# Kernel tuning notes

Hardware: AMD Instinct MI355X
Metric: run time of the kernel (lower is better)

The kernel has to match this reference:

```python
import jax, jax.numpy as jnp
import numpy as np

GRID_SIZE = 10
DEGREE = 3


def bspline_basis(x, grid_size=GRID_SIZE, degree=DEGREE):
    """Cox-de Boor B-spline basis on a uniform grid over [-1, 1].
    x: (...,) -> (..., grid_size + degree)
    """
    h = 2.0 / grid_size
    # extended knot vector, length grid_size + 2*degree + 1
    knots = jnp.arange(-degree, grid_size + degree + 1, dtype=x.dtype) * h - 1.0
    # keep inputs inside the grid support (standard KAN practice)
    x = jnp.clip(x, -1.0, 1.0 - 1e-6)
    xe = x[..., None]
    b = ((xe >= knots[:-1]) & (xe < knots[1:])).astype(x.dtype)  # degree-0, (..., K-1)
    for d in range(1, degree + 1):
        left = (xe - knots[: -(d + 1)]) / (knots[d:-1] - knots[: -(d + 1)]) * b[..., :-1]
        right = (knots[d + 1:] - xe) / (knots[d + 1:] - knots[1:-d]) * b[..., 1:]
        b = left + right
    return b  # (..., grid_size + degree)


def setup_inputs() -> dict:
    key = jax.random.key(0)
    k1, k2, k3 = jax.random.split(key, 3)
    B, S, IN, OUT, E = 4, 2048, 256, 256, 8
    n_basis = GRID_SIZE + DEGREE
    x = jax.random.normal(k1, (B, S, IN), dtype=jnp.float32)
    coeff = jax.random.normal(k2, (E, n_basis), dtype=jnp.float32) * 0.1
    gating_weights = jax.random.normal(k3, (IN, OUT, E), dtype=jnp.float32)
    return {"x": x, "coeff": coeff, "gating_weights": gating_weights}


def reference(x, coeff, gating_weights):
    # spline experts: elementwise basis eval, then per-expert linear combo
    basis = bspline_basis(x)                              # (B, S, I, n_basis)
    expert_outputs = jnp.einsum('bsin,en->bsie', basis, coeff)  # (B, S, I, E)
    gates = jax.nn.softmax(gating_weights, axis=-1)       # (I, O, E)
    out = jnp.einsum('bsie,ioe->bso', expert_outputs, gates)
    return out
```

## Files before the change

### kernel.cpp

```cpp
#include <hip/hip_runtime.h>

typedef __attribute__((ext_vector_type(8))) short short8;
typedef __attribute__((ext_vector_type(4))) float f32x4;

#define IN_DIM 256
#define OUT_DIM 256
#define NB 16
#define KDIM (IN_DIM * NB)
#define TM 128
#define TN 128
#define BK 64
#define LDA 72
#define KSPLIT 4
#define IPER (IN_DIM / KSPLIT)
#define STEPS (IPER / 4)

__device__ __forceinline__ unsigned short f2bf(float f) {
  union { float f; unsigned int u; } v; v.f = f;
  unsigned int r = v.u + 0x7fffu + ((v.u >> 16) & 1u);
  return (unsigned short)(r >> 16);
}

__device__ __forceinline__ void spline_row(float xv, unsigned short* rowp) {
  float xc = fminf(fmaxf(xv, -1.0f), 1.0f - 1e-6f);
  float u = (xc + 1.0f) * 5.0f;
  int c = (int)u;
  c = c > 9 ? 9 : (c < 0 ? 0 : c);
  float tt = u - (float)c;
  float omt = 1.0f - tt;
  float t2 = tt * tt, t3 = t2 * tt;
  float b0 = omt * omt * omt * (1.0f / 6.0f);
  float b1 = (3.0f * t3 - 6.0f * t2 + 4.0f) * (1.0f / 6.0f);
  float b2 = (-3.0f * t3 + 3.0f * t2 + 3.0f * tt + 1.0f) * (1.0f / 6.0f);
  float b3 = t3 * (1.0f / 6.0f);
  unsigned h0 = f2bf(b0), h1 = f2bf(b1), h2 = f2bf(b2), h3 = f2bf(b3);
  const int a = c >> 1;
  const bool odd = (c & 1) != 0;
  unsigned p01 = h0 | (h1 << 16);
  unsigned p23 = h2 | (h3 << 16);
  unsigned A0 = odd ? (h0 << 16) : p01;
  unsigned A1 = odd ? (h1 | (h2 << 16)) : p23;
  unsigned A2 = odd ? h3 : 0u;
  unsigned d[8];
#pragma unroll
  for (int j = 0; j < 8; ++j) {
    unsigned v = (j == a) ? A0 : 0u;
    v = (j == a + 1) ? A1 : v;
    v = (j == a + 2) ? A2 : v;
    d[j] = v;
  }
  *(int4*)&rowp[0] = *(const int4*)&d[0];
  *(int4*)&rowp[8] = *(const int4*)&d[4];
}

__global__ __launch_bounds__(256) void kan_prep(const float* __restrict__ coeff,
                                                const float* __restrict__ gw,
                                                unsigned short* __restrict__ BmT,
                                                float* __restrict__ out) {
  __shared__ float csh[104];
  __shared__ unsigned short tile[16][256];
  const int t = threadIdx.x;
  {
    const int bid = blockIdx.y * 16 + blockIdx.x;
    float4 z; z.x = z.y = z.z = z.w = 0.f;
    float4* ob = (float4*)out;
#pragma unroll
    for (int j = 0; j < 8; ++j) ob[(size_t)bid * 2048 + j * 256 + t] = z;
  }
  if (t < 104) csh[t] = coeff[t];
  __syncthreads();
  const int otile = blockIdx.x, itile = blockIdx.y;
  const int il = t >> 4, ol = t & 15;
  const int i = itile * 16 + il;
  const int o = otile * 16 + ol;
  const float* g = gw + (size_t)(i * OUT_DIM + o) * 8;
  float4 g0 = *(const float4*)g;
  float4 g1 = *(const float4*)(g + 4);
  float ge[8] = {g0.x, g0.y, g0.z, g0.w, g1.x, g1.y, g1.z, g1.w};
  float mx = ge[0];
#pragma unroll
  for (int e = 1; e < 8; ++e) mx = fmaxf(mx, ge[e]);
  float p[8]; float s = 0.f;
#pragma unroll
  for (int e = 0; e < 8; ++e) { p[e] = __expf(ge[e] - mx); s += p[e]; }
  const float inv = 1.0f / s;
  unsigned short row[16];
#pragma unroll
  for (int n = 0; n < 13; ++n) {
    float w = 0.f;
#pragma unroll
    for (int e = 0; e < 8; ++e) w += p[e] * csh[e * 13 + n];
    row[n] = f2bf(w * inv);
  }
  row[13] = 0; row[14] = 0; row[15] = 0;
  int4* dst = (int4*)&tile[ol][il * 16];
  dst[0] = *(const int4*)&row[0];
  dst[1] = *(const int4*)&row[8];
  __syncthreads();
  const int oo = t >> 4, ck = t & 15;
  int4 v0 = *(const int4*)&tile[oo][ck * 16];
  int4 v1 = *(const int4*)&tile[oo][ck * 16 + 8];
  int4* out4 = (int4*)(BmT + (size_t)(otile * 16 + oo) * KDIM + itile * 256 + ck * 16);
  out4[0] = v0;
  out4[1] = v1;
}

__global__ __launch_bounds__(256, 2) void kan_gemm(const float* __restrict__ x,
                                                   const unsigned short* __restrict__ BmT,
                                                   float* __restrict__ out) {
  __shared__ unsigned short AshB[2][TM * LDA];
  __shared__ unsigned short BshB[2][TN * LDA];

  const int t = threadIdx.x;
  const int lane = t & 63;
  const int wave = t >> 6;
  const int wm = wave & 1, wn = wave >> 1;
  const int mb = blockIdx.x * TM;
  const int ob = blockIdx.y * TN;
  const int i0 = blockIdx.z * IPER;

  const int r = t & 127;
  const int ph = t >> 7;
  const float* xrow = x + (size_t)(mb + r) * IN_DIM + i0 + 2 * ph;
  const int adst = r * LDA + 2 * ph * NB;

  const unsigned short* bsrc[4];
  int bdst[4];
#pragma unroll
  for (int q = 0; q < 4; ++q) {
    int olo = (t >> 3) + 32 * q;
    bsrc[q] = BmT + (size_t)(ob + olo) * KDIM + i0 * NB + (t & 7) * 8;
    bdst[q] = olo * LDA + (t & 7) * 8;
  }

  f32x4 acc[4][4];
#pragma unroll
  for (int a = 0; a < 4; ++a)
#pragma unroll
    for (int b = 0; b < 4; ++b) acc[a][b] = (f32x4){0.f, 0.f, 0.f, 0.f};

  int aoff[4], boff[4];
#pragma unroll
  for (int f = 0; f < 4; ++f) {
    aoff[f] = (wm * 64 + f * 16 + (lane & 15)) * LDA + (lane >> 4) * 8;
    boff[f] = (wn * 64 + f * 16 + (lane & 15)) * LDA + (lane >> 4) * 8;
  }

  float2 xs[STEPS];
#pragma unroll
  for (int s = 0; s < STEPS; ++s) xs[s] = *(const float2*)(xrow + 4 * s);

  {
    int4 breg[4];
#pragma unroll
    for (int q = 0; q < 4; ++q) breg[q] = *(const int4*)(bsrc[q]);
#pragma unroll
    for (int q = 0; q < 4; ++q) *(int4*)&BshB[0][bdst[q]] = breg[q];
    spline_row(xs[0].x, &AshB[0][adst]);
    spline_row(xs[0].y, &AshB[0][adst + NB]);
  }

#pragma unroll
  for (int s = 0; s < STEPS; ++s) {
    __syncthreads();
    const int cur = s & 1;
    const bool more = (s + 1 < STEPS);
    int4 breg[4];
    if (more) {
#pragma unroll
      for (int q = 0; q < 4; ++q) breg[q] = *(const int4*)(bsrc[q] + (s + 1) * BK);
    }
    const unsigned short* Ac = AshB[cur];
    const unsigned short* Bc = BshB[cur];
#pragma unroll
    for (int kc = 0; kc < 2; ++kc) {
      short8 af[4], bfr[4];
#pragma unroll
      for (int f = 0; f < 4; ++f) af[f] = *(const short8*)&Ac[aoff[f] + kc * 32];
#pragma unroll
      for (int f = 0; f < 4; ++f) bfr[f] = *(const short8*)&Bc[boff[f] + kc * 32];
#pragma unroll
      for (int mf = 0; mf < 4; ++mf)
#pragma unroll
        for (int nf = 0; nf < 4; ++nf)
          acc[mf][nf] = __builtin_amdgcn_mfma_f32_16x16x32_bf16(af[mf], bfr[nf], acc[mf][nf], 0, 0, 0);
    }
    if (more) {
      unsigned short* An = AshB[1 - cur];
      unsigned short* Bn = BshB[1 - cur];
#pragma unroll
      for (int q = 0; q < 4; ++q) *(int4*)&Bn[bdst[q]] = breg[q];
      spline_row(xs[s + 1].x, An + adst);
      spline_row(xs[s + 1].y, An + adst + NB);
    }
  }

#pragma unroll
  for (int mf = 0; mf < 4; ++mf)
#pragma unroll
    for (int nf = 0; nf < 4; ++nf)
#pragma unroll
      for (int q = 0; q < 4; ++q) {
        int row = mb + wm * 64 + mf * 16 + ((lane >> 4) << 2) + q;
        int col = ob + wn * 64 + nf * 16 + (lane & 15);
        atomicAdd(out + (size_t)row * OUT_DIM + col, acc[mf][nf][q]);
      }
}

extern "C" void kernel_launch(void* const* d_in, const int* in_sizes, int n_in,
                              void* d_out, int out_size, void* d_ws, size_t ws_size,
                              hipStream_t stream) {
  const float* x     = (const float*)d_in[0];
  const float* coeff = (const float*)d_in[1];
  const float* gw    = (const float*)d_in[2];
  float* out = (float*)d_out;
  unsigned short* BmT = (unsigned short*)d_ws;

  kan_prep<<<dim3(16, 16), dim3(256), 0, stream>>>(coeff, gw, BmT, out);
  dim3 grid(8192 / TM, OUT_DIM / TN, KSPLIT);
  kan_gemm<<<grid, dim3(256), 0, stream>>>(x, BmT, out);
}
```

Before: 114.2 us.

## Use 512-thread blocks with eight waves splitting the GEMM tile

The kan_gemm kernel now runs 512 threads (8 waves) per block instead of 256. Each wave computes a 32x64 sub-tile rather than 64x64, and the spline and B-tile staging work is spread over twice as many threads. The aim is more latency hiding and less per-thread register pressure, so more waves are resident per CU. In exchange, each wave reuses its loaded fragments less and the larger block makes barrier synchronisation more costly.

```diff
diff --git a/kernel.cpp b/kernel.cpp
--- a/kernel.cpp
+++ b/kernel.cpp
@@ -105,7 +105,7 @@
   out4[1] = v1;
 }
 
-__global__ __launch_bounds__(256, 2) void kan_gemm(const float* __restrict__ x,
+__global__ __launch_bounds__(512, 4) void kan_gemm(const float* __restrict__ x,
                                                    const unsigned short* __restrict__ BmT,
                                                    float* __restrict__ out) {
   __shared__ unsigned short AshB[2][TM * LDA];
@@ -114,50 +114,51 @@
   const int t = threadIdx.x;
   const int lane = t & 63;
   const int wave = t >> 6;
-  const int wm = wave & 1, wn = wave >> 1;
+  const int wn = wave & 1, wm = wave >> 1;
   const int mb = blockIdx.x * TM;
   const int ob = blockIdx.y * TN;
   const int i0 = blockIdx.z * IPER;
 
   const int r = t & 127;
-  const int ph = t >> 7;
-  const float* xrow = x + (size_t)(mb + r) * IN_DIM + i0 + 2 * ph;
-  const int adst = r * LDA + 2 * ph * NB;
-
-  const unsigned short* bsrc[4];
-  int bdst[4];
-#pragma unroll
-  for (int q = 0; q < 4; ++q) {
-    int olo = (t >> 3) + 32 * q;
-    bsrc[q] = BmT + (size_t)(ob + olo) * KDIM + i0 * NB + (t & 7) * 8;
-    bdst[q] = olo * LDA + (t & 7) * 8;
-  }
-
-  f32x4 acc[4][4];
-#pragma unroll
-  for (int a = 0; a < 4; ++a)
+  const int il = t >> 7;
+  const float* xrow = x + (size_t)(mb + r) * IN_DIM + i0 + il;
+  const int adst = r * LDA + il * NB;
+
+  const unsigned short* bsrc[2];
+  int bdst[2];
+#pragma unroll
+  for (int q = 0; q < 2; ++q) {
+    int id = t + q * 512;
+    int brow = id >> 3, pos = id & 7;
+    bsrc[q] = BmT + (size_t)(ob + brow) * KDIM + i0 * NB + pos * 8;
+    bdst[q] = brow * LDA + pos * 8;
+  }
+
+  f32x4 acc[2][4];
+#pragma unroll
+  for (int a = 0; a < 2; ++a)
 #pragma unroll
     for (int b = 0; b < 4; ++b) acc[a][b] = (f32x4){0.f, 0.f, 0.f, 0.f};
 
-  int aoff[4], boff[4];
-#pragma unroll
-  for (int f = 0; f < 4; ++f) {
-    aoff[f] = (wm * 64 + f * 16 + (lane & 15)) * LDA + (lane >> 4) * 8;
+  int aoff[2], boff[4];
+#pragma unroll
+  for (int f = 0; f < 2; ++f)
+    aoff[f] = (wm * 32 + f * 16 + (lane & 15)) * LDA + (lane >> 4) * 8;
+#pragma unroll
+  for (int f = 0; f < 4; ++f)
     boff[f] = (wn * 64 + f * 16 + (lane & 15)) * LDA + (lane >> 4) * 8;
-  }
-
-  float2 xs[STEPS];
-#pragma unroll
-  for (int s = 0; s < STEPS; ++s) xs[s] = *(const float2*)(xrow + 4 * s);
+
+  float xs[STEPS];
+#pragma unroll
+  for (int s = 0; s < STEPS; ++s) xs[s] = xrow[4 * s];
 
   {
-    int4 breg[4];
-#pragma unroll
-    for (int q = 0; q < 4; ++q) breg[q] = *(const int4*)(bsrc[q]);
-#pragma unroll
-    for (int q = 0; q < 4; ++q) *(int4*)&BshB[0][bdst[q]] = breg[q];
-    spline_row(xs[0].x, &AshB[0][adst]);
-    spline_row(xs[0].y, &AshB[0][adst + NB]);
+    int4 breg[2];
+#pragma unroll
+    for (int q = 0; q < 2; ++q) breg[q] = *(const int4*)(bsrc[q]);
+#pragma unroll
+    for (int q = 0; q < 2; ++q) *(int4*)&BshB[0][bdst[q]] = breg[q];
+    spline_row(xs[0], &AshB[0][adst]);
   }
 
 #pragma unroll
@@ -165,22 +166,22 @@
     __syncthreads();
     const int cur = s & 1;
     const bool more = (s + 1 < STEPS);
-    int4 breg[4];
+    int4 breg[2];
     if (more) {
 #pragma unroll
-      for (int q = 0; q < 4; ++q) breg[q] = *(const int4*)(bsrc[q] + (s + 1) * BK);
+      for (int q = 0; q < 2; ++q) breg[q] = *(const int4*)(bsrc[q] + (s + 1) * BK);
     }
     const unsigned short* Ac = AshB[cur];
     const unsigned short* Bc = BshB[cur];
 #pragma unroll
     for (int kc = 0; kc < 2; ++kc) {
-      short8 af[4], bfr[4];
-#pragma unroll
-      for (int f = 0; f < 4; ++f) af[f] = *(const short8*)&Ac[aoff[f] + kc * 32];
+      short8 af[2], bfr[4];
+#pragma unroll
+      for (int f = 0; f < 2; ++f) af[f] = *(const short8*)&Ac[aoff[f] + kc * 32];
 #pragma unroll
       for (int f = 0; f < 4; ++f) bfr[f] = *(const short8*)&Bc[boff[f] + kc * 32];
 #pragma unroll
-      for (int mf = 0; mf < 4; ++mf)
+      for (int mf = 0; mf < 2; ++mf)
 #pragma unroll
         for (int nf = 0; nf < 4; ++nf)
           acc[mf][nf] = __builtin_amdgcn_mfma_f32_16x16x32_bf16(af[mf], bfr[nf], acc[mf][nf], 0, 0, 0);
@@ -189,19 +190,18 @@
       unsigned short* An = AshB[1 - cur];
       unsigned short* Bn = BshB[1 - cur];
 #pragma unroll
-      for (int q = 0; q < 4; ++q) *(int4*)&Bn[bdst[q]] = breg[q];
-      spline_row(xs[s + 1].x, An + adst);
-      spline_row(xs[s + 1].y, An + adst + NB);
+      for (int q = 0; q < 2; ++q) *(int4*)&Bn[bdst[q]] = breg[q];
+      spline_row(xs[s + 1], An + adst);
     }
   }
 
 #pragma unroll
-  for (int mf = 0; mf < 4; ++mf)
+  for (int mf = 0; mf < 2; ++mf)
 #pragma unroll
     for (int nf = 0; nf < 4; ++nf)
 #pragma unroll
       for (int q = 0; q < 4; ++q) {
-        int row = mb + wm * 64 + mf * 16 + ((lane >> 4) << 2) + q;
+        int row = mb + wm * 32 + mf * 16 + ((lane >> 4) << 2) + q;
         int col = ob + wn * 64 + nf * 16 + (lane & 15);
         atomicAdd(out + (size_t)row * OUT_DIM + col, acc[mf][nf][q]);
       }
@@ -218,5 +218,5 @@
 
   kan_prep<<<dim3(16, 16), dim3(256), 0, stream>>>(coeff, gw, BmT, out);
   dim3 grid(8192 / TM, OUT_DIM / TN, KSPLIT);
-  kan_gemm<<<grid, dim3(256), 0, stream>>>(x, BmT, out);
-}
+  kan_gemm<<<grid, dim3(512), 0, stream>>>(x, BmT, out);
+}
```

Measured after the change: 118.5 us. 1.04x slower.
